# Kernel optimization log

Hardware: AMD Instinct MI355X
Metric: run time of the kernel (lower is better)

## Reference

```python
import jax, jax.numpy as jnp
import numpy as np

B, N, DIM, H = 2, 4096, 512, 8
DH = DIM // H  # head dim = 64


def setup_inputs() -> dict:
    key = jax.random.key(0)
    kx, kw, kb = jax.random.split(key, 3)
    x = jax.random.normal(kx, (B, N, DIM), dtype=jnp.float32)
    W = jax.random.normal(kw, (DIM, 3 * DIM), dtype=jnp.float32) / np.sqrt(DIM)
    b = jax.random.normal(kb, (3 * DIM,), dtype=jnp.float32) * 0.02
    return {"x": x, "W": W, "b": b}


def reference(x, W, b):
    Bx, n, d = x.shape
    qvk = x @ W + b  # [B, n, 3*dim]
    # torch.chunk order in source: q, v, k
    q, v, k = jnp.split(qvk, 3, axis=-1)

    def heads(t):  # [B, n, dim] -> [B, h, n, dh]
        return t.reshape(Bx, n, H, DH).transpose(0, 2, 1, 3)

    q, v, k = heads(q), heads(v), heads(k)
    # full (non-fused) attention: materializes [B, h, n, n] scores
    scale = jnp.einsum('bhqd,bhkd->bhqk', q, k) / jnp.sqrt(jnp.float32(DH))
    atn = jax.nn.softmax(scale, axis=-1)
    out = jnp.einsum('bhqk,bhkd->bhqd', atn, v)  # [B, h, n, dh]
    # concat_head: [B, h, n, dh] -> [B, n, h*dh]
    out = out.transpose(0, 2, 1, 3).reshape(Bx, n, H * DH)
    return out
```

## Files before the change

### kernel.cpp

```cpp
#include <hip/hip_runtime.h>
#include <hip/hip_bf16.h>
#include <math.h>

#define BB    2
#define NN    4096
#define DIM   512
#define NH    8
#define DH    64
#define NC    1536
#define MM    (BB*NN)

typedef __bf16 bf16x8 __attribute__((ext_vector_type(8)));
typedef __bf16 bf16x4 __attribute__((ext_vector_type(4)));
typedef float  f32x4  __attribute__((ext_vector_type(4)));

#define QSCALE 0.18033688011112042f

__device__ __forceinline__ int swz(int c) { return c ^ (((c >> 3) ^ (c >> 6)) & 7); }
__device__ __forceinline__ int kswz(int g) { return g ^ ((g >> 3) & 3) ^ (((g >> 6) & 1) << 2); }

__device__ __forceinline__ void gl_lds16(const __hip_bfloat16* g, __bf16* l) {
    __builtin_amdgcn_global_load_lds(
        (const __attribute__((address_space(1))) unsigned int*)g,
        (__attribute__((address_space(3))) unsigned int*)l, 16, 0, 0);
}

__device__ __forceinline__ int sniff(const unsigned short* x) {
    unsigned short v = x[2 * (threadIdx.x & 63)];
    int e = (v >> 7) & 0xFF;
    unsigned long long m = __ballot(e >= 110 && e <= 140);
    return __popcll(m) >= 48;
}

__device__ __forceinline__ f32x4 mfma32(bf16x8 a, bf16x8 b, f32x4 c) {
    return __builtin_amdgcn_mfma_f32_16x16x32_bf16(a, b, c, 0, 0, 0);
}

__global__ __launch_bounds__(256) void prep_kernel(
    const void* __restrict__ xin, const void* __restrict__ win,
    const void* __restrict__ bin,
    __hip_bfloat16* __restrict__ Xb, __hip_bfloat16* __restrict__ WT,
    float* __restrict__ Bf)
{
    __shared__ __bf16 tile[64][68];
    int bfmode = sniff((const unsigned short*)xin);
    int bid = blockIdx.x;
    int t = threadIdx.x;
    if (bid < 2048) {
        if (bfmode) return;
        int i = (bid * 256 + t) * 8;
        const float* xf = (const float*)xin + i;
        bf16x8 v;
        for (int j = 0; j < 8; j++) v[j] = (__bf16)xf[j];
        *(bf16x8*)(Xb + i) = v;
    } else if (bid < 2048 + 192) {
        int tl = bid - 2048;
        int kt = tl / 24, nt = tl % 24;
        int tx = t & 63, tyq = t >> 6;
        for (int r = 0; r < 16; r++) {
            int kl = r * 4 + tyq;
            int gi = (kt * 64 + kl) * NC + nt * 64 + tx;
            float v = bfmode ? __bfloat162float(((const __hip_bfloat16*)win)[gi])
                             : ((const float*)win)[gi];
            tile[kl][tx] = (__bf16)v;
        }
        __syncthreads();
        for (int r = 0; r < 16; r++) {
            int nl = r * 4 + tyq;
            WT[(size_t)(nt * 64 + nl) * DIM + kt * 64 + tx] = (__hip_bfloat16)(float)tile[tx][nl];
        }
    } else {
        int i = (bid - 2048 - 192) * 256 + t;
        if (i < NC)
            Bf[i] = bfmode ? __bfloat162float(((const __hip_bfloat16*)bin)[i])
                           : ((const float*)bin)[i];
    }
}

__global__ __launch_bounds__(256, 3) void qkv_gemm(
    const unsigned short* __restrict__ xs,
    const __hip_bfloat16* __restrict__ Xb,
    const __hip_bfloat16* __restrict__ WT,
    const float* __restrict__ Bf,
    __hip_bfloat16* __restrict__ Qb,
    __hip_bfloat16* __restrict__ Kb,
    __hip_bfloat16* __restrict__ Vt)
{
    __shared__ __align__(16) __bf16 smem[16384];
    __bf16* Xs = smem;
    __bf16* Ws = smem + 8192;

    int bfmode = sniff(xs);
    const __hip_bfloat16* X = bfmode ? (const __hip_bfloat16*)xs : Xb;

    int wave = threadIdx.x >> 6, lane = threadIdx.x & 63;
    int lane16 = lane & 15, quad = lane >> 4;
    int bm = blockIdx.x / 12, bn = blockIdx.x % 12;
    int m0b = bm * 128, n0b = bn * 128;
    int wm = wave >> 1, wn = wave & 1;
    int m0 = m0b + wm * 64, n0 = n0b + wn * 64;

    int xgo[2], sbase[2];
    for (int j = 0; j < 2; j++) {
        int p = (wave * 2 + j) * 64 + lane;
        int g = swz(p);
        xgo[j] = (g >> 2) * DIM + (g & 3) * 8;
        sbase[j] = (wave * 2 + j) * 512;
    }
    int aoff[4], boff[4];
    for (int mi = 0; mi < 4; mi++)
        aoff[mi] = swz((wm * 64 + mi * 16 + lane16) * 4 + quad) * 8;
    for (int ni = 0; ni < 4; ni++)
        boff[ni] = swz((wn * 64 + ni * 16 + lane16) * 4 + quad) * 8;

    const __hip_bfloat16* Xg = X  + (size_t)m0b * DIM;
    const __hip_bfloat16* Wg = WT + (size_t)n0b * DIM;

    for (int j = 0; j < 2; j++) {
        gl_lds16(Xg + xgo[j], &Xs[sbase[j]]);
        gl_lds16(Wg + xgo[j], &Ws[sbase[j]]);
    }
    __syncthreads();

    f32x4 acc[4][4] = {};
    for (int k0 = 0; k0 < DIM; k0 += 32) {
        int cur = (k0 >> 5) & 1, nbuf = cur ^ 1;
        int k1 = (k0 + 32) & (DIM - 1);
        for (int j = 0; j < 2; j++) {
            gl_lds16(Xg + k1 + xgo[j], &Xs[nbuf * 4096 + sbase[j]]);
            gl_lds16(Wg + k1 + xgo[j], &Ws[nbuf * 4096 + sbase[j]]);
        }
        bf16x8 a[4], b[4];
        for (int mi = 0; mi < 4; mi++) a[mi] = *(const bf16x8*)&Xs[cur * 4096 + aoff[mi]];
        for (int ni = 0; ni < 4; ni++) b[ni] = *(const bf16x8*)&Ws[cur * 4096 + boff[ni]];
        for (int mi = 0; mi < 4; mi++)
            for (int ni = 0; ni < 4; ni++)
                acc[mi][ni] = mfma32(a[mi], b[ni], acc[mi][ni]);
        __syncthreads();
    }
    __bf16* epi = smem + wave * 4096;

    int sec = n0b >> 9;
    int bidx = m0b >> 12;
    if (sec == 1) {
        for (int ni = 0; ni < 4; ni++) {
            int nloc = ni * 16 + lane16;
            float bv = Bf[n0 + nloc];
            for (int mi = 0; mi < 4; mi++) {
                bf16x4 pk;
                for (int r = 0; r < 4; r++) pk[r] = (__bf16)(acc[mi][ni][r] + bv);
                int idx = swz(nloc * 8 + mi * 2 + (quad >> 1)) * 8 + (quad & 1) * 4;
                *(bf16x4*)&epi[idx] = pk;
            }
        }
        int hl = (n0 - 512) >> 6;
        int mbase = m0b - bidx * NN + wm * 64;
        for (int p = 0; p < 8; p++) {
            int n = p * 8 + (lane >> 3), mc = lane & 7;
            bf16x8 vv = *(const bf16x8*)&epi[swz(n * 8 + mc) * 8];
            *(bf16x8*)(Vt + ((size_t)(bidx * 8 + hl) * 64 + n) * NN + mbase + mc * 8) = vv;
        }
    } else {
        bool isQ = (sec == 0);
        int h = (n0 & 511) >> 6;
        for (int mi = 0; mi < 4; mi++) {
            for (int ni = 0; ni < 4; ni++) {
                float bv = Bf[n0 + ni * 16 + lane16];
                int dl = ni * 16 + lane16;
                for (int r = 0; r < 4; r++) {
                    int row = mi * 16 + quad * 4 + r;
                    float v = acc[mi][ni][r] + bv;
                    if (isQ) v *= QSCALE;
                    epi[swz(row * 8 + (dl >> 3)) * 8 + (dl & 7)] = (__bf16)v;
                }
            }
        }
        __hip_bfloat16* dst = isQ ? Qb : Kb;
        int bh = bidx * 8 + h;
        int mbase = m0 - bidx * NN;
        for (int p = 0; p < 8; p++) {
            int row = p * 8 + (lane >> 3), dc = lane & 7;
            bf16x8 vv = *(const bf16x8*)&epi[swz(row * 8 + dc) * 8];
            *(bf16x8*)(dst + ((size_t)bh * NN + mbase + row) * DH + dc * 8) = vv;
        }
    }
}

__global__ __launch_bounds__(256, 2) void attn_fused(
    const __hip_bfloat16* __restrict__ Qb,
    const __hip_bfloat16* __restrict__ Kb,
    const __hip_bfloat16* __restrict__ Vt,
    void* __restrict__ OutV,
    const unsigned short* __restrict__ xs)
{
    __shared__ __align__(16) __bf16 smem[26624];

    int bfmode = sniff(xs);
    int wave = threadIdx.x >> 6, lane = threadIdx.x & 63;
    int lane16 = lane & 15, quad = lane >> 4;
    int half = wave >> 1, qw = wave & 1;

    int orig = blockIdx.x;
    int nbid = (orig & 7) * 64 + (orig >> 3);
    int bh = nbid >> 5;
    int qt = nbid & 31;
    int q0 = qt * 128 + qw * 64;
    int khbase = half * 2048;

    __bf16* Kst = smem + half * 8192;
    __bf16* Vst = smem + half * 8192 + 4096;

    const __hip_bfloat16* Qh = Qb + (size_t)bh * NN * DH;
    const __hip_bfloat16* Kh = Kb + (size_t)bh * NN * DH;
    const __hip_bfloat16* Vh = Vt + (size_t)bh * DH * NN;

    bf16x8 bq[4][2];
    #pragma unroll
    for (int qf = 0; qf < 4; qf++)
        #pragma unroll
        for (int kc = 0; kc < 2; kc++)
            bq[qf][kc] = *(const bf16x8*)(Qh + (size_t)(q0 + qf * 16 + lane16) * DH + kc * 32 + quad * 8);

    int kgo[4], vgo[4], sbase[4];
    #pragma unroll
    for (int j = 0; j < 4; j++) {
        int p = j * 64 + lane;
        int gk = kswz(p);
        kgo[j] = (gk >> 3) * DH + (gk & 7) * 8;
        int gv = swz(p);
        vgo[j] = (gv >> 2) * NN + (gv & 3) * 8;
        sbase[j] = j * 512;
    }
    int koff[2][2];
    #pragma unroll
    for (int kf = 0; kf < 2; kf++) {
        int key = (lane16 >> 2) * 8 + 4 * kf + (lane16 & 3);
        #pragma unroll
        for (int kc = 0; kc < 2; kc++)
            koff[kf][kc] = kswz(key * 8 + kc * 4 + quad) * 8;
    }
    int voff[4];
    #pragma unroll
    for (int dt = 0; dt < 4; dt++)
        voff[dt] = swz((dt * 16 + lane16) * 4 + quad) * 8;

    for (int j = 0; j < 4; j++) {
        gl_lds16(Kh + (size_t)khbase * DH + kgo[j], &Kst[sbase[j]]);
        gl_lds16(Vh + khbase + vgo[j], &Vst[sbase[j]]);
    }
    __syncthreads();

    bf16x8 ones8;
    #pragma unroll
    for (int j = 0; j < 8; j++) ones8[j] = (__bf16)1.0f;
    f32x4 o[4][4] = {};
    f32x4 ol[4] = {};

    for (int it = 0; it < 64; ++it) {
        int cur = it & 1, nb = cur ^ 1;
        int k1 = khbase + ((it + 1) & 63) * 32;
        for (int j = 0; j < 4; j++) {
            gl_lds16(Kh + (size_t)k1 * DH + kgo[j], &Kst[nb * 2048 + sbase[j]]);
            gl_lds16(Vh + k1 + vgo[j], &Vst[nb * 2048 + sbase[j]]);
        }

        bf16x8 ka[2][2];
        #pragma unroll
        for (int kf = 0; kf < 2; kf++)
            #pragma unroll
            for (int kc = 0; kc < 2; kc++)
                ka[kf][kc] = *(const bf16x8*)&Kst[cur * 2048 + koff[kf][kc]];
        f32x4 s[2][4];
        #pragma unroll
        for (int kf = 0; kf < 2; kf++)
            #pragma unroll
            for (int qf = 0; qf < 4; qf++) {
                f32x4 t = {};
                t = mfma32(ka[kf][0], bq[qf][0], t);
                t = mfma32(ka[kf][1], bq[qf][1], t);
                s[kf][qf] = t;
            }

        bf16x4 pt[2][4];
        #pragma unroll
        for (int kf = 0; kf < 2; kf++)
            #pragma unroll
            for (int qf = 0; qf < 4; qf++)
                #pragma unroll
                for (int r = 0; r < 4; r++)
                    pt[kf][qf][r] = (__bf16)__builtin_amdgcn_exp2f(s[kf][qf][r]);

        bf16x8 av[4];
        #pragma unroll
        for (int dt = 0; dt < 4; dt++)
            av[dt] = *(const bf16x8*)&Vst[cur * 2048 + voff[dt]];
        #pragma unroll
        for (int qf = 0; qf < 4; qf++) {
            bf16x8 pb = __builtin_shufflevector(pt[0][qf], pt[1][qf],
                                                0, 1, 2, 3, 4, 5, 6, 7);
            #pragma unroll
            for (int dt = 0; dt < 4; dt++)
                o[dt][qf] = mfma32(av[dt], pb, o[dt][qf]);
            ol[qf] = mfma32(ones8, pb, ol[qf]);
        }

        __syncthreads();
    }

    float* Osh = (float*)smem;
    float* lsh = Osh + 128 * 68;
    if (half == 1) {
        #pragma unroll
        for (int qf = 0; qf < 4; qf++) {
            #pragma unroll
            for (int dt = 0; dt < 4; dt++)
                *(f32x4*)&Osh[(qw * 64 + qf * 16 + lane16) * 68 + dt * 16 + quad * 4] = o[dt][qf];
            if (quad == 0) lsh[qw * 64 + qf * 16 + lane16] = ol[qf][0];
        }
    }
    __syncthreads();
    if (half == 0) {
        __bf16* epi = smem + 17664 + qw * 4096;
        #pragma unroll
        for (int qf = 0; qf < 4; qf++) {
            float l = ol[qf][0] + lsh[qw * 64 + qf * 16 + lane16];
            float rinv = 1.0f / l;
            #pragma unroll
            for (int dt = 0; dt < 4; dt++) {
                f32x4 po = *(const f32x4*)&Osh[(qw * 64 + qf * 16 + lane16) * 68 + dt * 16 + quad * 4];
                #pragma unroll
                for (int r = 0; r < 4; r++) {
                    int d = dt * 16 + quad * 4 + r;
                    int row = qf * 16 + lane16;
                    epi[swz(row * 8 + (d >> 3)) * 8 + (d & 7)] = (__bf16)((o[dt][qf][r] + po[r]) * rinv);
                }
            }
        }
        int bidx = bh >> 3, h = bh & 7;
        for (int p = 0; p < 8; p++) {
            int row = p * 8 + (lane >> 3), mc = lane & 7;
            bf16x8 vv = *(const bf16x8*)&epi[swz(row * 8 + mc) * 8];
            size_t base = ((size_t)bidx * NN + q0 + row) * DIM + h * 64 + mc * 8;
            if (bfmode) {
                *(bf16x8*)((__hip_bfloat16*)OutV + base) = vv;
            } else {
                float* op = (float*)OutV + base;
                f32x4 f0, f1;
                for (int j = 0; j < 4; j++) { f0[j] = (float)vv[j]; f1[j] = (float)vv[4 + j]; }
                *(f32x4*)op = f0;
                *(f32x4*)(op + 4) = f1;
            }
        }
    }
}

extern "C" void kernel_launch(void* const* d_in, const int* in_sizes, int n_in,
                              void* d_out, int out_size, void* d_ws, size_t ws_size,
                              hipStream_t stream) {
    char* ws = (char*)d_ws;
    __hip_bfloat16* Qb = (__hip_bfloat16*)ws;
    __hip_bfloat16* Kb = Qb + (size_t)BB * NH * NN * DH;
    __hip_bfloat16* Vt = Kb + (size_t)BB * NH * NN * DH;
    __hip_bfloat16* WT = Vt + (size_t)BB * NH * NN * DH;
    __hip_bfloat16* Xb = WT + (size_t)NC * DIM;
    float* Bf = (float*)(Xb + (size_t)MM * DIM);

    prep_kernel<<<2048 + 192 + 6, 256, 0, stream>>>(d_in[0], d_in[1], d_in[2], Xb, WT, Bf);
    qkv_gemm<<<(MM / 128) * (NC / 128), 256, 0, stream>>>(
        (const unsigned short*)d_in[0], Xb, WT, Bf, Qb, Kb, Vt);
    attn_fused<<<512, 256, 0, stream>>>(Qb, Kb, Vt, d_out, (const unsigned short*)d_in[0]);
}
```

Before: 176.2 us.

## Triple-buffer K/V tiles with split loads and relaxed waitcnt barriers

Moves the attention loop's K/V staging from double to triple buffering in LDS, prefetching two tiles ahead. The two waves that share a key half now split each tile's loads between them. __syncthreads is replaced by an explicit s_waitcnt vmcnt(4) plus s_barrier, so the tile after next can stay in flight across the barrier. The V fragment reads are hoisted next to the K reads and the MFMA blocks are wrapped in s_setprio. The extra buffer raises LDS use per half, and the hand-tuned waitcnt count depends on the exact number of loads each lane issues.

```diff
diff --git a/kernel.cpp b/kernel.cpp
--- a/kernel.cpp
+++ b/kernel.cpp
@@ -207,8 +207,8 @@
     int q0 = qt * 128 + qw * 64;
     int khbase = half * 2048;
 
-    __bf16* Kst = smem + half * 8192;
-    __bf16* Vst = smem + half * 8192 + 4096;
+    __bf16* Kst = smem + half * 12288;
+    __bf16* Vst = Kst + 6144;
 
     const __hip_bfloat16* Qh = Qb + (size_t)bh * NN * DH;
     const __hip_bfloat16* Kh = Kb + (size_t)bh * NN * DH;
@@ -221,15 +221,15 @@
         for (int kc = 0; kc < 2; kc++)
             bq[qf][kc] = *(const bf16x8*)(Qh + (size_t)(q0 + qf * 16 + lane16) * DH + kc * 32 + quad * 8);
 
-    int kgo[4], vgo[4], sbase[4];
-    #pragma unroll
-    for (int j = 0; j < 4; j++) {
-        int p = j * 64 + lane;
+    int kgo[2], vgo[2], sbase[2];
+    #pragma unroll
+    for (int j = 0; j < 2; j++) {
+        int p = (qw * 2 + j) * 64 + lane;
         int gk = kswz(p);
         kgo[j] = (gk >> 3) * DH + (gk & 7) * 8;
         int gv = swz(p);
         vgo[j] = (gv >> 2) * NN + (gv & 3) * 8;
-        sbase[j] = j * 512;
+        sbase[j] = (qw * 2 + j) * 512;
     }
     int koff[2][2];
     #pragma unroll
@@ -244,11 +244,19 @@
     for (int dt = 0; dt < 4; dt++)
         voff[dt] = swz((dt * 16 + lane16) * 4 + quad) * 8;
 
-    for (int j = 0; j < 4; j++) {
-        gl_lds16(Kh + (size_t)khbase * DH + kgo[j], &Kst[sbase[j]]);
-        gl_lds16(Vh + khbase + vgo[j], &Vst[sbase[j]]);
-    }
-    __syncthreads();
+    #pragma unroll
+    for (int t = 0; t < 2; t++) {
+        int kt = khbase + t * 32;
+        #pragma unroll
+        for (int j = 0; j < 2; j++) {
+            gl_lds16(Kh + (size_t)kt * DH + kgo[j], &Kst[t * 2048 + sbase[j]]);
+            gl_lds16(Vh + kt + vgo[j], &Vst[t * 2048 + sbase[j]]);
+        }
+    }
+    asm volatile("s_waitcnt vmcnt(0)" ::: "memory");
+    __builtin_amdgcn_sched_barrier(0);
+    __builtin_amdgcn_s_barrier();
+    __builtin_amdgcn_sched_barrier(0);
 
     bf16x8 ones8;
     #pragma unroll
@@ -256,12 +264,13 @@
     f32x4 o[4][4] = {};
     f32x4 ol[4] = {};
 
+    int cur = 0, pf = 2;
     for (int it = 0; it < 64; ++it) {
-        int cur = it & 1, nb = cur ^ 1;
-        int k1 = khbase + ((it + 1) & 63) * 32;
-        for (int j = 0; j < 4; j++) {
-            gl_lds16(Kh + (size_t)k1 * DH + kgo[j], &Kst[nb * 2048 + sbase[j]]);
-            gl_lds16(Vh + k1 + vgo[j], &Vst[nb * 2048 + sbase[j]]);
+        int kt = khbase + ((it + 2) & 63) * 32;
+        #pragma unroll
+        for (int j = 0; j < 2; j++) {
+            gl_lds16(Kh + (size_t)kt * DH + kgo[j], &Kst[pf * 2048 + sbase[j]]);
+            gl_lds16(Vh + kt + vgo[j], &Vst[pf * 2048 + sbase[j]]);
         }
 
         bf16x8 ka[2][2];
@@ -270,7 +279,13 @@
             #pragma unroll
             for (int kc = 0; kc < 2; kc++)
                 ka[kf][kc] = *(const bf16x8*)&Kst[cur * 2048 + koff[kf][kc]];
+        bf16x8 av[4];
+        #pragma unroll
+        for (int dt = 0; dt < 4; dt++)
+            av[dt] = *(const bf16x8*)&Vst[cur * 2048 + voff[dt]];
+
         f32x4 s[2][4];
+        __builtin_amdgcn_s_setprio(1);
         #pragma unroll
         for (int kf = 0; kf < 2; kf++)
             #pragma unroll
@@ -280,6 +295,7 @@
                 t = mfma32(ka[kf][1], bq[qf][1], t);
                 s[kf][qf] = t;
             }
+        __builtin_amdgcn_s_setprio(0);
 
         bf16x4 pt[2][4];
         #pragma unroll
@@ -290,10 +306,7 @@
                 for (int r = 0; r < 4; r++)
                     pt[kf][qf][r] = (__bf16)__builtin_amdgcn_exp2f(s[kf][qf][r]);
 
-        bf16x8 av[4];
-        #pragma unroll
-        for (int dt = 0; dt < 4; dt++)
-            av[dt] = *(const bf16x8*)&Vst[cur * 2048 + voff[dt]];
+        __builtin_amdgcn_s_setprio(1);
         #pragma unroll
         for (int qf = 0; qf < 4; qf++) {
             bf16x8 pb = __builtin_shufflevector(pt[0][qf], pt[1][qf],
@@ -303,9 +316,21 @@
                 o[dt][qf] = mfma32(av[dt], pb, o[dt][qf]);
             ol[qf] = mfma32(ones8, pb, ol[qf]);
         }
-
-        __syncthreads();
-    }
+        __builtin_amdgcn_s_setprio(0);
+
+        asm volatile("s_waitcnt vmcnt(4) lgkmcnt(0)" ::: "memory");
+        __builtin_amdgcn_sched_barrier(0);
+        __builtin_amdgcn_s_barrier();
+        __builtin_amdgcn_sched_barrier(0);
+
+        cur = (cur == 2) ? 0 : cur + 1;
+        pf  = (pf  == 2) ? 0 : pf + 1;
+    }
+
+    asm volatile("s_waitcnt vmcnt(0) lgkmcnt(0)" ::: "memory");
+    __builtin_amdgcn_sched_barrier(0);
+    __builtin_amdgcn_s_barrier();
+    __builtin_amdgcn_sched_barrier(0);
 
     float* Osh = (float*)smem;
     float* lsh = Osh + 128 * 68;
```

Result: faster. 165.0 us (median of 2 runs) (-6.3%).

## Give each wave private K/V LDS buffers and drop per-iteration block barriers

Applied to the files above, without the earlier changes.

Each wave now stages its own double-buffered K/V tiles in LDS instead of two waves sharing one buffer per key half. This lets the per-iteration __syncthreads be replaced by a wave-local s_waitcnt vmcnt on the async global-to-LDS loads. The V fragment reads are hoisted ahead of the QK MFMAs, and s_setprio is raised around the MFMA sections. In exchange, LDS per block grows to 64 KB, which could limit occupancy.

```diff
diff --git a/kernel.cpp b/kernel.cpp
--- a/kernel.cpp
+++ b/kernel.cpp
@@ -193,7 +193,7 @@
     void* __restrict__ OutV,
     const unsigned short* __restrict__ xs)
 {
-    __shared__ __align__(16) __bf16 smem[26624];
+    __shared__ __align__(16) __bf16 smem[32768];
 
     int bfmode = sniff(xs);
     int wave = threadIdx.x >> 6, lane = threadIdx.x & 63;
@@ -207,8 +207,8 @@
     int q0 = qt * 128 + qw * 64;
     int khbase = half * 2048;
 
-    __bf16* Kst = smem + half * 8192;
-    __bf16* Vst = smem + half * 8192 + 4096;
+    __bf16* Kst = smem + wave * 8192;
+    __bf16* Vst = Kst + 4096;
 
     const __hip_bfloat16* Qh = Qb + (size_t)bh * NN * DH;
     const __hip_bfloat16* Kh = Kb + (size_t)bh * NN * DH;
@@ -221,7 +221,7 @@
         for (int kc = 0; kc < 2; kc++)
             bq[qf][kc] = *(const bf16x8*)(Qh + (size_t)(q0 + qf * 16 + lane16) * DH + kc * 32 + quad * 8);
 
-    int kgo[4], vgo[4], sbase[4];
+    int kgo[4], vgo[4];
     #pragma unroll
     for (int j = 0; j < 4; j++) {
         int p = j * 64 + lane;
@@ -229,7 +229,6 @@
         kgo[j] = (gk >> 3) * DH + (gk & 7) * 8;
         int gv = swz(p);
         vgo[j] = (gv >> 2) * NN + (gv & 3) * 8;
-        sbase[j] = j * 512;
     }
     int koff[2][2];
     #pragma unroll
@@ -244,11 +243,13 @@
     for (int dt = 0; dt < 4; dt++)
         voff[dt] = swz((dt * 16 + lane16) * 4 + quad) * 8;
 
+    #pragma unroll
     for (int j = 0; j < 4; j++) {
-        gl_lds16(Kh + (size_t)khbase * DH + kgo[j], &Kst[sbase[j]]);
-        gl_lds16(Vh + khbase + vgo[j], &Vst[sbase[j]]);
-    }
-    __syncthreads();
+        gl_lds16(Kh + (size_t)khbase * DH + kgo[j], &Kst[j * 512]);
+        gl_lds16(Vh + khbase + vgo[j], &Vst[j * 512]);
+    }
+    asm volatile("s_waitcnt vmcnt(0)" ::: "memory");
+    __builtin_amdgcn_sched_barrier(0);
 
     bf16x8 ones8;
     #pragma unroll
@@ -256,13 +257,18 @@
     f32x4 o[4][4] = {};
     f32x4 ol[4] = {};
 
+    int cur = 0;
     for (int it = 0; it < 64; ++it) {
-        int cur = it & 1, nb = cur ^ 1;
-        int k1 = khbase + ((it + 1) & 63) * 32;
+        int nb = cur ^ 1;
+        int kt = khbase + ((it + 1) & 63) * 32;
+        #pragma unroll
         for (int j = 0; j < 4; j++) {
-            gl_lds16(Kh + (size_t)k1 * DH + kgo[j], &Kst[nb * 2048 + sbase[j]]);
-            gl_lds16(Vh + k1 + vgo[j], &Vst[nb * 2048 + sbase[j]]);
-        }
+            gl_lds16(Kh + (size_t)kt * DH + kgo[j], &Kst[nb * 2048 + j * 512]);
+            gl_lds16(Vh + kt + vgo[j], &Vst[nb * 2048 + j * 512]);
+        }
+
+        asm volatile("s_waitcnt vmcnt(8)" ::: "memory");
+        __builtin_amdgcn_sched_barrier(0);
 
         bf16x8 ka[2][2];
         #pragma unroll
@@ -270,7 +276,13 @@
             #pragma unroll
             for (int kc = 0; kc < 2; kc++)
                 ka[kf][kc] = *(const bf16x8*)&Kst[cur * 2048 + koff[kf][kc]];
+        bf16x8 av[4];
+        #pragma unroll
+        for (int dt = 0; dt < 4; dt++)
+            av[dt] = *(const bf16x8*)&Vst[cur * 2048 + voff[dt]];
+
         f32x4 s[2][4];
+        __builtin_amdgcn_s_setprio(1);
         #pragma unroll
         for (int kf = 0; kf < 2; kf++)
             #pragma unroll
@@ -280,6 +292,7 @@
                 t = mfma32(ka[kf][1], bq[qf][1], t);
                 s[kf][qf] = t;
             }
+        __builtin_amdgcn_s_setprio(0);
 
         bf16x4 pt[2][4];
         #pragma unroll
@@ -290,10 +303,7 @@
                 for (int r = 0; r < 4; r++)
                     pt[kf][qf][r] = (__bf16)__builtin_amdgcn_exp2f(s[kf][qf][r]);
 
-        bf16x8 av[4];
-        #pragma unroll
-        for (int dt = 0; dt < 4; dt++)
-            av[dt] = *(const bf16x8*)&Vst[cur * 2048 + voff[dt]];
+        __builtin_amdgcn_s_setprio(1);
         #pragma unroll
         for (int qf = 0; qf < 4; qf++) {
             bf16x8 pb = __builtin_shufflevector(pt[0][qf], pt[1][qf],
@@ -303,9 +313,17 @@
                 o[dt][qf] = mfma32(av[dt], pb, o[dt][qf]);
             ol[qf] = mfma32(ones8, pb, ol[qf]);
         }
-
-        __syncthreads();
-    }
+        __builtin_amdgcn_s_setprio(0);
+
+        __builtin_amdgcn_sched_barrier(0);
+
+        cur = nb;
+    }
+
+    asm volatile("s_waitcnt vmcnt(0) lgkmcnt(0)" ::: "memory");
+    __builtin_amdgcn_sched_barrier(0);
+    __builtin_amdgcn_s_barrier();
+    __builtin_amdgcn_sched_barrier(0);
 
     float* Osh = (float*)smem;
     float* lsh = Osh + 128 * 68;
```

New measurement: 174.5 us. About the same (-1.0%).
